# Kernel tuning notes

Measured on AMD Instinct MI355X. Metric: run time of the kernel, lower is better.

Reference implementation:

```python
import jax, jax.numpy as jnp
import numpy as np

K = 256
Q = 64
T = 500001  # length of return series r


def setup_inputs() -> dict:
    key = jax.random.key(0)
    k_r, k_b, k_w0, k_w = jax.random.split(key, 4)
    r = 0.01 * jax.random.normal(k_r, (T,), dtype=jnp.float32)
    a0 = jnp.float32(0.0)
    a1 = jnp.float32(0.0)
    raw_beta0 = jnp.float32(-4.0)
    raw_beta = (-4.0 + 0.1 * jax.random.normal(k_b, (K,))).astype(jnp.float32)
    raw_w0 = (-8.0 + 0.1 * jax.random.normal(k_w0, (K,))).astype(jnp.float32)
    raw_w = (-4.0 + 0.1 * jax.random.normal(k_w, (K, Q))).astype(jnp.float32)
    return {"r": r, "a0": a0, "a1": a1, "raw_beta0": raw_beta0,
            "raw_beta": raw_beta, "raw_w0": raw_w0, "raw_w": raw_w}


def reference(r, a0, a1, raw_beta0, raw_beta, raw_w0, raw_w):
    # AR(1) residuals
    u = r[1:] - a0 - a1 * r[:-1]          # [T-1]
    u2 = u * u                            # [T-1]
    n = u.shape[0]
    # init_u2 = unbiased variance of u2, repeated q times (torch.var default ddof=1)
    init_u2 = jnp.full((Q,), jnp.var(u2, ddof=1), dtype=u2.dtype)
    u2_full = jnp.concatenate([init_u2, u2])  # [q + T-1]
    # vectorized windowing: row t holds u2_full[t+q-1], ..., u2_full[t] (flipped window)
    t_idx = jnp.arange(n)[:, None]        # [n,1]
    lag_idx = jnp.arange(Q)[None, :]      # [1,q]
    idx = (Q + t_idx) - 1 - lag_idx       # [n,q]
    u2_lags = u2_full[idx]                # [n,q]
    # softplus-MLP volatility
    w0 = jax.nn.softplus(raw_w0)          # [k]
    w = jax.nn.softplus(raw_w)            # [k,q]
    h = jax.nn.relu(w0[None, :] + u2_lags @ w.T)  # [n,k]
    beta0 = jax.nn.softplus(raw_beta0)
    beta = jax.nn.softplus(raw_beta)      # [k]
    sigma2 = beta0 + h @ beta + 1e-8      # [n]
    # Gaussian negative log-likelihood
    nll = (0.5 * n * jnp.log(jnp.float32(2.0 * np.pi))
           + 0.5 * jnp.sum(jnp.log(sigma2))
           + 0.5 * jnp.sum(u2 / sigma2))
    return nll
```

## Files before the change

kernel.cpp:

```cpp
#include <hip/hip_runtime.h>
#include <math.h>

#define K_ 256
#define Q_ 64
#define NT 500000
#define NTILES (NT / 16)
#define TT_ 32
#define GRID_MAIN ((NTILES + TT_ - 1) / TT_)
#define NSUM 245

#define WS_BETA0  2
#define WS_U2B0   4
#define U2ELEMS   (Q_ + NT + 16)
#define U2F       ((U2ELEMS + 1) / 2)
#define WS_U2B1   (WS_U2B0 + U2F)
#define WS_BPACK  (WS_U2B1 + U2F)
#define WS_W0     (WS_BPACK + 8192)
#define WS_BETA   (WS_W0 + K_)
#define WS_PART   (WS_BETA + K_)
#define WS_PART2  (WS_PART + 512)
#define WS_OUT    (WS_PART2 + 512)
#define WS_CNT    (WS_OUT + 1024)

typedef __attribute__((ext_vector_type(8))) __bf16 bf16x8;
typedef __attribute__((ext_vector_type(4))) float  f32x4;

__device__ __forceinline__ float softplusf(float x) {
    return (x > 20.f) ? x : log1pf(__expf(x));
}

__device__ __forceinline__ unsigned short f2bf(float f) {
    unsigned int u = __float_as_uint(f);
    u = u + 0x7FFFu + ((u >> 16) & 1u);
    return (unsigned short)(u >> 16);
}

__global__ void k_sum(const float* __restrict__ r,
                      const float* __restrict__ a0p,
                      const float* __restrict__ a1p,
                      float* __restrict__ ws) {
    __shared__ float red[8];
    int i0 = (blockIdx.x * 256 + threadIdx.x) * 8;
    float a0 = a0p[0], a1 = a1p[0];
    float v = 0.f, v2 = 0.f;
    if (i0 < NT) {
        float rr[9];
        *(float4*)&rr[0] = *(const float4*)(r + i0);
        *(float4*)&rr[4] = *(const float4*)(r + i0 + 4);
        rr[8] = r[i0 + 8];
        unsigned short bs[8];
        #pragma unroll
        for (int j = 0; j < 8; ++j) {
            float u  = rr[j + 1] - a0 - a1 * rr[j];
            float u2 = u * u;
            bs[j] = f2bf(u2);
            v += u2;
            v2 = fmaf(u2, u2, v2);
        }
        unsigned short* b0 = (unsigned short*)(ws + WS_U2B0);
        unsigned short* b1 = (unsigned short*)(ws + WS_U2B1);
        __builtin_memcpy(b0 + Q_ + i0, bs, 16);
        b1[Q_ - 1 + i0] = bs[0];
        __builtin_memcpy(b1 + Q_ + i0, bs + 1, 12);
        b1[Q_ + i0 + 6] = bs[7];
    }
    #pragma unroll
    for (int off = 32; off > 0; off >>= 1) {
        v  += __shfl_down(v,  off, 64);
        v2 += __shfl_down(v2, off, 64);
    }
    int wv = threadIdx.x >> 6;
    if ((threadIdx.x & 63) == 0) { red[wv * 2] = v; red[wv * 2 + 1] = v2; }
    __syncthreads();
    if (threadIdx.x == 0) {
        ws[WS_PART  + blockIdx.x] = red[0] + red[2] + red[4] + red[6];
        ws[WS_PART2 + blockIdx.x] = red[1] + red[3] + red[5] + red[7];
    }
}

__global__ void k_prep(const float* __restrict__ raw_beta0,
                       const float* __restrict__ raw_beta,
                       const float* __restrict__ raw_w0,
                       const float* __restrict__ raw_w,
                       float* __restrict__ ws) {
    int idx = blockIdx.x * blockDim.x + threadIdx.x;
    if (idx < 16384) {
        int jj = idx & 7, l = (idx >> 3) & 63, s = (idx >> 9) & 1, kc = idx >> 10;
        int j    = 32 * s + 8 * (l >> 4) + jj;
        int kout = kc * 16 + (l & 15);
        ((unsigned short*)(ws + WS_BPACK))[idx] =
            f2bf(softplusf(raw_w[kout * Q_ + (Q_ - 1 - j)]));
    } else if (idx < 16384 + K_) {
        int k = idx - 16384;
        ws[WS_W0 + k] = softplusf(raw_w0[k]);
    } else if (idx < 16384 + 2 * K_) {
        int k = idx - (16384 + K_);
        ws[WS_BETA + k] = softplusf(raw_beta[k]);
    } else if (idx < 16384 + 2 * K_ + Q_) {
        int j = idx - (16384 + 2 * K_);
        float s1 = 0.f, s2 = 0.f;
        #pragma unroll
        for (int p = j; p < NSUM; p += 64) {
            s1 += ws[WS_PART  + p];
            s2 += ws[WS_PART2 + p];
        }
        #pragma unroll
        for (int mask = 1; mask < 64; mask <<= 1) {
            s1 += __shfl_xor(s1, mask, 64);
            s2 += __shfl_xor(s2, mask, 64);
        }
        float n  = (float)NT;
        float var = (s2 - s1 * s1 / n) / (n - 1.f);
        unsigned short b = f2bf(var);
        ((unsigned short*)(ws + WS_U2B0))[j] = b;
        if (j < Q_ - 1) ((unsigned short*)(ws + WS_U2B1))[j] = b;
        if (j == 0) ws[WS_BETA0] = softplusf(raw_beta0[0]);
    }
}

__global__ void
__attribute__((amdgpu_flat_work_group_size(256, 256)))
__attribute__((amdgpu_waves_per_eu(4, 4)))
k_main(const float* __restrict__ r,
       const float* __restrict__ a0p,
       const float* __restrict__ a1p,
       float* __restrict__ ws, float* __restrict__ out) {
    __shared__ __align__(16) float sig[TT_ * 256];
    __shared__ float red[4];
    __shared__ int lastflag;

    int tid = threadIdx.x;
    int l = tid & 63, w = tid >> 6;
    int m = l & 15, q = l >> 4;

    const unsigned short* bp = (const unsigned short*)(ws + WS_BPACK);
    float beta0v = ws[WS_BETA0];
    float a0 = a0p[0], a1 = a1p[0];

    bf16x8 Wf[4][2];
    f32x4 w0c[4], betc[4];
    #pragma unroll
    for (int i = 0; i < 4; ++i) {
        int kc = w * 4 + i;
        #pragma unroll
        for (int s = 0; s < 2; ++s)
            __builtin_memcpy(&Wf[i][s], bp + ((kc * 2 + s) * 64 + l) * 8, 16);
        w0c[i]  = *(const f32x4*)(ws + WS_W0   + kc * 16 + q * 4);
        betc[i] = *(const f32x4*)(ws + WS_BETA + kc * 16 + q * 4);
    }

    int par = m & 1;
    const char* abase = (const char*)(ws + (par ? WS_U2B1 : WS_U2B0));
    int aoff = (blockIdx.x * 512 + m + 8 * q - par) * 2;

    bf16x8 F0, F1, F2, F3;
    __builtin_memcpy(&F0, abase + aoff,      16);
    __builtin_memcpy(&F1, abase + aoff + 32, 16);
    __builtin_memcpy(&F2, abase + aoff + 64, 16);
    __builtin_memcpy(&F3, abase + aoff + 96, 16);

    #define TILE_BODY(U0v, U1v, LD, nofs)                                     \
        {                                                                     \
            bf16x8 Ld_;                                                       \
            __builtin_memcpy(&Ld_, abase + aoff + (nofs), 16);                \
            float p[4];                                                       \
            _Pragma("unroll")                                                 \
            for (int i = 0; i < 4; ++i) {                                     \
                f32x4 acc = __builtin_amdgcn_mfma_f32_16x16x32_bf16(          \
                    Wf[i][0], U0v, w0c[i], 0, 0, 0);                          \
                acc = __builtin_amdgcn_mfma_f32_16x16x32_bf16(                \
                    Wf[i][1], U1v, acc, 0, 0, 0);                             \
                float pi;                                                     \
                pi = betc[i][0] * fmaxf(acc[0], 0.f);                         \
                pi = fmaf(betc[i][1], fmaxf(acc[1], 0.f), pi);                \
                pi = fmaf(betc[i][2], fmaxf(acc[2], 0.f), pi);                \
                pi = fmaf(betc[i][3], fmaxf(acc[3], 0.f), pi);                \
                p[i] = pi;                                                    \
            }                                                                 \
            sig[it * 256 + tid] = (p[0] + p[1]) + (p[2] + p[3]);              \
            LD = Ld_;                                                         \
        }

    #pragma unroll 1
    for (int it4 = 0; it4 < TT_ / 4; ++it4) {
        bf16x8 L0, L1, L2, L3;
        int it;
        it = it4 * 4;     TILE_BODY(F0, F2, L0, 128)
        it = it4 * 4 + 1; TILE_BODY(F1, F3, L1, 160)
        it = it4 * 4 + 2; TILE_BODY(F2, L0, L2, 192)
        it = it4 * 4 + 3; TILE_BODY(F3, L1, L3, 224)
        F0 = L0; F1 = L1; F2 = L2; F3 = L3;
        aoff += 128;
    }
    #undef TILE_BODY

    __syncthreads();

    float val = 0.f;
    #pragma unroll
    for (int rep = 0; rep < 2; ++rep) {
        int lt = tid + rep * 256;
        int tile = lt >> 4, tt = lt & 15;
        const float* sp = &sig[tile * 256 + tt];
        float s = 0.f;
        #pragma unroll
        for (int wq = 0; wq < 16; ++wq) s += sp[wq * 16];
        float sg = beta0v + s + 1e-8f;
        int t = blockIdx.x * 512 + lt;
        if (t < NT) {
            float u  = r[t + 1] - a0 - a1 * r[t];
            val += __logf(sg) + (u * u) / sg;
        }
    }
    #pragma unroll
    for (int mask = 1; mask < 64; mask <<= 1)
        val += __shfl_xor(val, mask, 64);
    if (l == 0) red[w] = val;
    __syncthreads();

    if (tid == 0) {
        ws[WS_OUT + blockIdx.x] = red[0] + red[1] + red[2] + red[3];
        __threadfence();
        unsigned old = atomicAdd((unsigned*)(ws + WS_CNT), 1u);
        lastflag = (old == GRID_MAIN - 1);
    }
    __syncthreads();
    if (lastflag) {
        __threadfence();
        float s = 0.f;
        for (int p = tid; p < GRID_MAIN; p += 256) s += ws[WS_OUT + p];
        #pragma unroll
        for (int mask = 1; mask < 64; mask <<= 1)
            s += __shfl_xor(s, mask, 64);
        if (l == 0) red[w] = s;
        __syncthreads();
        if (tid == 0)
            out[0] = 0.5f * (float)NT * 1.8378770664093453f
                   + 0.5f * (red[0] + red[1] + red[2] + red[3]);
    }
}

extern "C" void kernel_launch(void* const* d_in, const int* in_sizes, int n_in,
                              void* d_out, int out_size, void* d_ws, size_t ws_size,
                              hipStream_t stream) {
    const float* r        = (const float*)d_in[0];
    const float* a0       = (const float*)d_in[1];
    const float* a1       = (const float*)d_in[2];
    const float* raw_b0   = (const float*)d_in[3];
    const float* raw_beta = (const float*)d_in[4];
    const float* raw_w0   = (const float*)d_in[5];
    const float* raw_w    = (const float*)d_in[6];
    float* out = (float*)d_out;
    float* ws  = (float*)d_ws;

    hipMemsetAsync(ws + WS_CNT, 0, 4, stream);

    k_sum<<<NSUM, 256, 0, stream>>>(r, a0, a1, ws);

    int prep_threads = 16384 + 2 * K_ + Q_;
    k_prep<<<(prep_threads + 255) / 256, 256, 0, stream>>>(
        raw_b0, raw_beta, raw_w0, raw_w, ws);

    k_main<<<GRID_MAIN, 256, 0, stream>>>(r, a0, a1, ws, out);
}
```

Baseline: 106.4 us.

## Split hidden units across eight waves per block and halve tiles per block

The main kernel now uses 512-thread blocks in which each of eight waves handles two 16-unit chunks of K instead of four, and each block covers 16 time tiles instead of 32. That roughly doubles the grid and removes the fixed waves_per_eu setting. The aim is to raise wave-level parallelism and occupancy and to cut per-wave register pressure. In exchange, every wave in a block reloads the same u2 fragments, the LDS reduction per timestep sums 32 partials, and the final cross-block reduction has twice as many entries.

```diff
diff --git a/kernel.cpp b/kernel.cpp
--- a/kernel.cpp
+++ b/kernel.cpp
@@ -5,7 +5,7 @@
 #define Q_ 64
 #define NT 500000
 #define NTILES (NT / 16)
-#define TT_ 32
+#define TT_ 16
 #define GRID_MAIN ((NTILES + TT_ - 1) / TT_)
 #define NSUM 245
 
@@ -20,7 +20,7 @@
 #define WS_PART   (WS_BETA + K_)
 #define WS_PART2  (WS_PART + 512)
 #define WS_OUT    (WS_PART2 + 512)
-#define WS_CNT    (WS_OUT + 1024)
+#define WS_CNT    (WS_OUT + 2048)
 
 typedef __attribute__((ext_vector_type(8))) __bf16 bf16x8;
 typedef __attribute__((ext_vector_type(4))) float  f32x4;
@@ -119,14 +119,13 @@
 }
 
 __global__ void
-__attribute__((amdgpu_flat_work_group_size(256, 256)))
-__attribute__((amdgpu_waves_per_eu(4, 4)))
+__attribute__((amdgpu_flat_work_group_size(512, 512)))
 k_main(const float* __restrict__ r,
        const float* __restrict__ a0p,
        const float* __restrict__ a1p,
        float* __restrict__ ws, float* __restrict__ out) {
-    __shared__ __align__(16) float sig[TT_ * 256];
-    __shared__ float red[4];
+    __shared__ __align__(16) float sig[TT_ * 512];
+    __shared__ float red[8];
     __shared__ int lastflag;
 
     int tid = threadIdx.x;
@@ -137,11 +136,11 @@
     float beta0v = ws[WS_BETA0];
     float a0 = a0p[0], a1 = a1p[0];
 
-    bf16x8 Wf[4][2];
-    f32x4 w0c[4], betc[4];
+    bf16x8 Wf[2][2];
+    f32x4 w0c[2], betc[2];
     #pragma unroll
-    for (int i = 0; i < 4; ++i) {
-        int kc = w * 4 + i;
+    for (int i = 0; i < 2; ++i) {
+        int kc = w * 2 + i;
         #pragma unroll
         for (int s = 0; s < 2; ++s)
             __builtin_memcpy(&Wf[i][s], bp + ((kc * 2 + s) * 64 + l) * 8, 16);
@@ -151,7 +150,7 @@
 
     int par = m & 1;
     const char* abase = (const char*)(ws + (par ? WS_U2B1 : WS_U2B0));
-    int aoff = (blockIdx.x * 512 + m + 8 * q - par) * 2;
+    int aoff = (blockIdx.x * 256 + m + 8 * q - par) * 2;
 
     bf16x8 F0, F1, F2, F3;
     __builtin_memcpy(&F0, abase + aoff,      16);
@@ -163,21 +162,24 @@
         {                                                                     \
             bf16x8 Ld_;                                                       \
             __builtin_memcpy(&Ld_, abase + aoff + (nofs), 16);                \
-            float p[4];                                                       \
-            _Pragma("unroll")                                                 \
-            for (int i = 0; i < 4; ++i) {                                     \
-                f32x4 acc = __builtin_amdgcn_mfma_f32_16x16x32_bf16(          \
-                    Wf[i][0], U0v, w0c[i], 0, 0, 0);                          \
-                acc = __builtin_amdgcn_mfma_f32_16x16x32_bf16(                \
-                    Wf[i][1], U1v, acc, 0, 0, 0);                             \
-                float pi;                                                     \
-                pi = betc[i][0] * fmaxf(acc[0], 0.f);                         \
-                pi = fmaf(betc[i][1], fmaxf(acc[1], 0.f), pi);                \
-                pi = fmaf(betc[i][2], fmaxf(acc[2], 0.f), pi);                \
-                pi = fmaf(betc[i][3], fmaxf(acc[3], 0.f), pi);                \
-                p[i] = pi;                                                    \
-            }                                                                 \
-            sig[it * 256 + tid] = (p[0] + p[1]) + (p[2] + p[3]);              \
+            float p0, p1;                                                     \
+            f32x4 acc0 = __builtin_amdgcn_mfma_f32_16x16x32_bf16(             \
+                Wf[0][0], U0v, w0c[0], 0, 0, 0);                              \
+            acc0 = __builtin_amdgcn_mfma_f32_16x16x32_bf16(                   \
+                Wf[0][1], U1v, acc0, 0, 0, 0);                                \
+            f32x4 acc1 = __builtin_amdgcn_mfma_f32_16x16x32_bf16(             \
+                Wf[1][0], U0v, w0c[1], 0, 0, 0);                              \
+            acc1 = __builtin_amdgcn_mfma_f32_16x16x32_bf16(                   \
+                Wf[1][1], U1v, acc1, 0, 0, 0);                                \
+            p0 = betc[0][0] * fmaxf(acc0[0], 0.f);                            \
+            p0 = fmaf(betc[0][1], fmaxf(acc0[1], 0.f), p0);                   \
+            p0 = fmaf(betc[0][2], fmaxf(acc0[2], 0.f), p0);                   \
+            p0 = fmaf(betc[0][3], fmaxf(acc0[3], 0.f), p0);                   \
+            p1 = betc[1][0] * fmaxf(acc1[0], 0.f);                            \
+            p1 = fmaf(betc[1][1], fmaxf(acc1[1], 0.f), p1);                   \
+            p1 = fmaf(betc[1][2], fmaxf(acc1[2], 0.f), p1);                   \
+            p1 = fmaf(betc[1][3], fmaxf(acc1[3], 0.f), p1);                   \
+            sig[it * 512 + tid] = p0 + p1;                                    \
             LD = Ld_;                                                         \
         }
 
@@ -197,19 +199,17 @@
     __syncthreads();
 
     float val = 0.f;
-    #pragma unroll
-    for (int rep = 0; rep < 2; ++rep) {
-        int lt = tid + rep * 256;
-        int tile = lt >> 4, tt = lt & 15;
-        const float* sp = &sig[tile * 256 + tt];
+    if (tid < 256) {
+        int tile = tid >> 4, tt = tid & 15;
+        const float* sp = &sig[tile * 512 + tt];
         float s = 0.f;
         #pragma unroll
-        for (int wq = 0; wq < 16; ++wq) s += sp[wq * 16];
+        for (int c = 0; c < 32; ++c) s += sp[c * 16];
         float sg = beta0v + s + 1e-8f;
-        int t = blockIdx.x * 512 + lt;
+        int t = blockIdx.x * 256 + tid;
         if (t < NT) {
             float u  = r[t + 1] - a0 - a1 * r[t];
-            val += __logf(sg) + (u * u) / sg;
+            val = __logf(sg) + (u * u) / sg;
         }
     }
     #pragma unroll
@@ -219,7 +219,7 @@
     __syncthreads();
 
     if (tid == 0) {
-        ws[WS_OUT + blockIdx.x] = red[0] + red[1] + red[2] + red[3];
+        ws[WS_OUT + blockIdx.x] = (red[0] + red[1]) + (red[2] + red[3]);
         __threadfence();
         unsigned old = atomicAdd((unsigned*)(ws + WS_CNT), 1u);
         lastflag = (old == GRID_MAIN - 1);
@@ -228,7 +228,7 @@
     if (lastflag) {
         __threadfence();
         float s = 0.f;
-        for (int p = tid; p < GRID_MAIN; p += 256) s += ws[WS_OUT + p];
+        for (int p = tid; p < GRID_MAIN; p += 512) s += ws[WS_OUT + p];
         #pragma unroll
         for (int mask = 1; mask < 64; mask <<= 1)
             s += __shfl_xor(s, mask, 64);
@@ -236,7 +236,8 @@
         __syncthreads();
         if (tid == 0)
             out[0] = 0.5f * (float)NT * 1.8378770664093453f
-                   + 0.5f * (red[0] + red[1] + red[2] + red[3]);
+                   + 0.5f * (((red[0] + red[1]) + (red[2] + red[3]))
+                           + ((red[4] + red[5]) + (red[6] + red[7])));
     }
 }
 
@@ -261,5 +262,5 @@
     k_prep<<<(prep_threads + 255) / 256, 256, 0, stream>>>(
         raw_b0, raw_beta, raw_w0, raw_w, ws);
 
-    k_main<<<GRID_MAIN, 256, 0, stream>>>(r, a0, a1, ws, out);
-}
+    k_main<<<GRID_MAIN, 512, 0, stream>>>(r, a0, a1, ws, out);
+}
```

New measurement: 131.3 us. +23.4%, slower.
